# Optimization experiments

Hardware: AMD Instinct MI355X
Metric: run time of the kernel (lower is better)

Reference implementation:

```python
import jax, jax.numpy as jnp
import numpy as np

N = 50000        # n_nodes
E = 640000       # n_edges
D = 128          # d_model (in_dim == out_dim)
H = 8            # num_heads
DH = D // H      # head dim = 16
EPS = 1e-5


def _batchnorm(x, g, b):
    # BatchNorm1d, training-mode batch statistics (biased variance)
    mu = jnp.mean(x, axis=0)
    var = jnp.mean((x - mu) ** 2, axis=0)
    return (x - mu) * jax.lax.rsqrt(var + EPS) * g + b


def setup_inputs() -> dict:
    key = jax.random.key(0)
    ks = jax.random.split(key, 16)
    s = 0.05
    h = jax.random.normal(ks[0], (N, D), jnp.float32)
    src = jax.random.randint(ks[1], (E,), 0, N)
    # guarantee every node has >= 1 incoming edge (avoids z == 0)
    dst = jnp.concatenate([jnp.arange(N), jax.random.randint(ks[2], (E - N,), 0, N)])
    return {
        "h": h,
        "src": src,
        "dst": dst,
        "WQ": jax.random.normal(ks[3], (D, D), jnp.float32) * s,
        "WK": jax.random.normal(ks[4], (D, D), jnp.float32) * s,
        "WV": jax.random.normal(ks[5], (D, D), jnp.float32) * s,
        "WO": jax.random.normal(ks[6], (D, D), jnp.float32) * s,
        "bO": jnp.zeros((D,), jnp.float32),
        "W1": jax.random.normal(ks[7], (2 * D, D), jnp.float32) * s,
        "b1": jnp.zeros((2 * D,), jnp.float32),
        "W2": jax.random.normal(ks[8], (D, 2 * D), jnp.float32) * s,
        "b2": jnp.zeros((D,), jnp.float32),
        "bn1_g": jnp.ones((D,), jnp.float32),
        "bn1_b": jnp.zeros((D,), jnp.float32),
        "bn2_g": jnp.ones((D,), jnp.float32),
        "bn2_b": jnp.zeros((D,), jnp.float32),
    }


def reference(h, src, dst, WQ, WK, WV, WO, bO, W1, b1, W2, b2, bn1_g, bn1_b, bn2_g, bn2_b):
    n = h.shape[0]
    # projections -> [N, H, DH]
    Q = (h @ WQ.T).reshape(n, H, DH)
    K = (h @ WK.T).reshape(n, H, DH)
    V = (h @ WV.T).reshape(n, H, DH)
    # per-edge score: sum(K[src] * Q[dst]) -> [E, H]; clamp/exp (scaled_exp)
    score = jnp.sum(K[src] * Q[dst], axis=-1) / np.sqrt(DH)
    score = jnp.exp(jnp.clip(score, -5.0, 5.0))
    # scatter-sum weighted values and normalizers to destination nodes
    wV = jax.ops.segment_sum(V[src] * score[..., None], dst, num_segments=n)  # [N,H,DH]
    z = jax.ops.segment_sum(score, dst, num_segments=n)                       # [N,H]
    attn = (wV / z[..., None]).reshape(n, D)
    # O projection + residual + BN1
    h1 = _batchnorm(h + (attn @ WO.T + bO), bn1_g, bn1_b)
    # FFN + residual + BN2
    f = jax.nn.relu(h1 @ W1.T + b1) @ W2.T + b2
    return _batchnorm(h1 + f, bn2_g, bn2_b)
```

## Files before the change

### kernel.cpp

```cpp
#include <hip/hip_runtime.h>
#include <math.h>


#define ND128 16384
typedef _Float16 f16;
typedef __attribute__((ext_vector_type(8))) _Float16 h8;
typedef __attribute__((ext_vector_type(4))) _Float16 h4;
typedef __attribute__((ext_vector_type(2))) _Float16 h2;
typedef __attribute__((ext_vector_type(4))) float f4;
typedef __attribute__((ext_vector_type(2))) float ff2;

__device__ __forceinline__ ff2 fp8x2_dec(unsigned v) {
#if __has_builtin(__builtin_amdgcn_cvt_pk_f32_fp8)
    return __builtin_amdgcn_cvt_pk_f32_fp8((int)v, false);
#else
    ff2 r;
    unsigned b0 = v & 0xffu, b1 = (v >> 8) & 0xffu;
    {
        unsigned e = (b0 >> 3) & 15u, m = b0 & 7u;
        float x = e ? __uint_as_float(((e + 120u) << 23) | (m << 20)) : (float)m * 0.001953125f;
        r.x = (b0 & 0x80u) ? -x : x;
    }
    {
        unsigned e = (b1 >> 3) & 15u, m = b1 & 7u;
        float x = e ? __uint_as_float(((e + 120u) << 23) | (m << 20)) : (float)m * 0.001953125f;
        r.y = (b1 & 0x80u) ? -x : x;
    }
    return r;
#endif
}

__device__ __forceinline__ ff2 dec_lo(unsigned v) {
#if __has_builtin(__builtin_amdgcn_cvt_pk_f32_fp8)
    return __builtin_amdgcn_cvt_pk_f32_fp8((int)v, false);
#else
    return fp8x2_dec(v & 0xffffu);
#endif
}
__device__ __forceinline__ ff2 dec_hi(unsigned v) {
#if __has_builtin(__builtin_amdgcn_cvt_pk_f32_fp8)
    return __builtin_amdgcn_cvt_pk_f32_fp8((int)v, true);
#else
    return fp8x2_dec((v >> 16) & 0xffffu);
#endif
}

#if !__has_builtin(__builtin_amdgcn_cvt_pk_fp8_f32)
__device__ __forceinline__ unsigned char fp8_1(float f) {
    float a = fabsf(f);
    unsigned sg = (__float_as_uint(f) >> 31) << 7;
    if (a >= 448.f) return (unsigned char)(sg | 0x7E);
    if (a < 0.0009765625f) return (unsigned char)sg;
    int E; float m = frexpf(a, &E);
    if (E - 1 < -6) {
        int q = (int)rintf(a * 512.f);
        if (q > 7) return (unsigned char)(sg | 0x08);
        return (unsigned char)(sg | q);
    }
    int q = (int)rintf(m * 16.f);
    if (q == 16) { q = 8; E += 1; }
    int Ef = E - 1 + 7;
    if (Ef > 15) return (unsigned char)(sg | 0x7E);
    return (unsigned char)(sg | (Ef << 3) | (q - 8));
}
#endif

__device__ __forceinline__ unsigned fp8_pack4(float a0, float a1, float a2, float a3) {
#if __has_builtin(__builtin_amdgcn_cvt_pk_fp8_f32)
    int pk = __builtin_amdgcn_cvt_pk_fp8_f32(a0, a1, 0, false);
    pk = __builtin_amdgcn_cvt_pk_fp8_f32(a2, a3, pk, true);
    return (unsigned)pk;
#else
    return (unsigned)fp8_1(a0) | ((unsigned)fp8_1(a1) << 8) |
           ((unsigned)fp8_1(a2) << 16) | ((unsigned)fp8_1(a3) << 24);
#endif
}

__global__ __launch_bounds__(256) void k_prep(
    const float* __restrict__ h, f16* __restrict__ hb,
    const float* __restrict__ WQ, const float* __restrict__ WK,
    const float* __restrict__ WV, const float* __restrict__ WO,
    const float* __restrict__ W2,
    f16* __restrict__ Wqb, f16* __restrict__ Wkb,
    f16* __restrict__ Wvb, f16* __restrict__ Wob, f16* __restrict__ W2b,
    float* __restrict__ bn, int* __restrict__ cursor, int N)
{
    const int slab = blockIdx.x, my = blockIdx.y;
    const int tid = threadIdx.x;
    if (my == 0) {
        if (tid < 128) {
            int ci = slab * 128 + tid;
            if (ci < N) cursor[ci] = 0;
        }
        if (slab == 6) { bn[tid] = 0.f; bn[tid + 256] = 0.f; }
    }
#pragma unroll
    for (int it2 = 0; it2 < 4; ++it2) {
        int it = my * 4 + it2;
        int cid = it * 256 + tid;
        int lane = cid & 63;
        int m = (cid >> 6) & 7;
        int kb = cid >> 9;
        int row = slab * 128 + m * 16 + (lane & 15);
        int col = kb * 32 + (lane >> 4) * 8;
        f16 o8[8];
        if (row < N) {
            const float* p = h + (size_t)row * 128 + col;
            float4 f0 = *(const float4*)p;
            float4 f1 = *(const float4*)(p + 4);
            o8[0] = (f16)f0.x; o8[1] = (f16)f0.y; o8[2] = (f16)f0.z; o8[3] = (f16)f0.w;
            o8[4] = (f16)f1.x; o8[5] = (f16)f1.y; o8[6] = (f16)f1.z; o8[7] = (f16)f1.w;
        } else {
#pragma unroll
            for (int j = 0; j < 8; ++j) o8[j] = (f16)0.f;
        }
        *(h8*)(hb + (size_t)slab * ND128 + (size_t)cid * 8) = *(const h8*)o8;
    }
    if (slab < 6 && my == 1) {
        const float* Wsrc; f16* dst; int K, base;
        if (slab < 4) {
            Wsrc = slab == 0 ? WQ : slab == 1 ? WK : slab == 2 ? WV : WO;
            dst  = slab == 0 ? Wqb : slab == 1 ? Wkb : slab == 2 ? Wvb : Wob;
            K = 128; base = 0;
        } else {
            Wsrc = W2; dst = W2b; K = 256; base = (slab - 4) * 2048;
        }
#pragma unroll
        for (int it = 0; it < 8; ++it) {
            int cid = base + it * 256 + tid;
            int lane = cid & 63;
            int kb, nt;
            if (K == 128) { kb = (cid >> 6) & 3; nt = cid >> 8; }
            else          { kb = (cid >> 6) & 7; nt = cid >> 9; }
            int row = nt * 16 + (lane & 15);
            int col = kb * 32 + (lane >> 4) * 8;
            const float* p = Wsrc + (size_t)row * K + col;
            f16 o8[8];
#pragma unroll
            for (int j = 0; j < 8; ++j) o8[j] = (f16)p[j];
            *(h8*)(dst + (size_t)cid * 8) = *(const h8*)o8;
        }
    }
}

__global__ __launch_bounds__(256) void k_qkv(
    const f16* __restrict__ hb, const f16* __restrict__ Wqb,
    const f16* __restrict__ Wkb, const f16* __restrict__ Wvb,
    f16* __restrict__ Qb, unsigned char* __restrict__ Kb8,
    unsigned char* __restrict__ Vb8, int N)
{
    const int slab = blockIdx.x, oidx = blockIdx.y, mh = blockIdx.z;
    const int w = threadIdx.x >> 6, lane = threadIdx.x & 63;
    const f16* __restrict__ Wb = oidx == 0 ? Wqb : oidx == 1 ? Wkb : Wvb;
    const f16* A = hb + (size_t)slab * ND128;

    h8 bfr[2][4];
#pragma unroll
    for (int nt = 0; nt < 2; ++nt)
#pragma unroll
        for (int kb = 0; kb < 4; ++kb)
            bfr[nt][kb] = *(const h8*)(Wb + (size_t)(((2 * w + nt) * 4 + kb) * 64 + lane) * 8);

    f4 acc[4][2];
    f4 zero = {0.f, 0.f, 0.f, 0.f};
#pragma unroll
    for (int m = 0; m < 4; ++m) { acc[m][0] = zero; acc[m][1] = zero; }

#pragma unroll
    for (int m = 0; m < 4; ++m) {
        int mg = mh * 4 + m;
#pragma unroll
        for (int kb = 0; kb < 4; ++kb) {
            h8 a = *(const h8*)(A + (size_t)((kb * 8 + mg) * 64 + lane) * 8);
            acc[m][0] = __builtin_amdgcn_mfma_f32_16x16x32_f16(bfr[0][kb], a, acc[m][0], 0, 0, 0);
            acc[m][1] = __builtin_amdgcn_mfma_f32_16x16x32_f16(bfr[1][kb], a, acc[m][1], 0, 0, 0);
        }
    }

    const int rl = lane & 15, quad = lane >> 4;
    if (oidx == 0) {
#pragma unroll
        for (int m = 0; m < 4; ++m) {
            int gr = slab * 128 + (mh * 4 + m) * 16 + rl;
            if (gr < N) {
#pragma unroll
                for (int nt = 0; nt < 2; ++nt) {
                    h4 o;
                    o[0] = (f16)acc[m][nt][0]; o[1] = (f16)acc[m][nt][1];
                    o[2] = (f16)acc[m][nt][2]; o[3] = (f16)acc[m][nt][3];
                    *(h4*)(Qb + (size_t)gr * 128 + w * 32 + nt * 16 + quad * 4) = o;
                }
            }
        }
    } else {
        unsigned char* __restrict__ O8 = oidx == 1 ? Kb8 : Vb8;
#pragma unroll
        for (int m = 0; m < 4; ++m) {
            int gr = slab * 128 + (mh * 4 + m) * 16 + rl;
            if (gr < N) {
#pragma unroll
                for (int nt = 0; nt < 2; ++nt) {
                    unsigned pk = fp8_pack4(acc[m][nt][0], acc[m][nt][1],
                                            acc[m][nt][2], acc[m][nt][3]);
                    *(unsigned*)(O8 + (size_t)gr * 128 + w * 32 + nt * 16 + quad * 4) = pk;
                }
            }
        }
    }
}

__global__ __launch_bounds__(256) void k_hist(
    const int* __restrict__ dst, int* __restrict__ cursor, int E)
{
    int e = blockIdx.x * 256 + threadIdx.x;
    if (e < E) atomicAdd(&cursor[dst[e]], 1);
}

__global__ __launch_bounds__(256) void k_scanA(
    const int* __restrict__ cnt, int* __restrict__ bsum, int N)
{
    const int t = threadIdx.x;
    int base = blockIdx.x * 2048 + t * 8;
    int s = 0;
#pragma unroll
    for (int j = 0; j < 8; ++j) {
        int idx = base + j;
        if (idx < N) s += cnt[idx];
    }
#pragma unroll
    for (int off = 32; off; off >>= 1) s += __shfl_down(s, off, 64);
    __shared__ int ws4[4];
    if ((t & 63) == 0) ws4[t >> 6] = s;
    __syncthreads();
    if (t == 0) bsum[blockIdx.x] = ws4[0] + ws4[1] + ws4[2] + ws4[3];
}

__global__ __launch_bounds__(256) void k_scanC(
    const int* __restrict__ cnt, const int* __restrict__ bsum,
    int* __restrict__ rowptr, int* __restrict__ cursor, int N, int nsb)
{
    const int t = threadIdx.x, b = blockIdx.x;
    __shared__ int sboff;
    if (t == 0) {
        int r = 0;
        for (int i2 = 0; i2 < b; ++i2) r += bsum[i2];
        sboff = r;
    }
    if (t == 64 && b == nsb - 1) {
        int r = 0;
        for (int i2 = 0; i2 < nsb; ++i2) r += bsum[i2];
        rowptr[N] = r;
    }
    int base = b * 2048 + t * 8;
    int loc[8];
    int s = 0;
#pragma unroll
    for (int j = 0; j < 8; ++j) {
        int idx = base + j;
        loc[j] = (idx < N) ? cnt[idx] : 0;
        s += loc[j];
    }
    __shared__ int part[256];
    part[t] = s;
    __syncthreads();
    for (int off = 1; off < 256; off <<= 1) {
        int v = (t >= off) ? part[t - off] : 0;
        __syncthreads();
        part[t] += v;
        __syncthreads();
    }
    int run = sboff + (t ? part[t - 1] : 0);
#pragma unroll
    for (int j = 0; j < 8; ++j) {
        int idx = base + j;
        if (idx < N) { rowptr[idx] = run; cursor[idx] = run; run += loc[j]; }
    }
}

__global__ __launch_bounds__(256) void k_scatter(
    const int* __restrict__ src, const int* __restrict__ dst,
    int* __restrict__ cursor, int* __restrict__ csr_src, int E)
{
    int e = blockIdx.x * 256 + threadIdx.x;
    if (e < E) {
        int pos = atomicAdd(&cursor[dst[e]], 1);
        csr_src[pos] = src[e];
    }
}

__global__ __launch_bounds__(256) void k_attn(
    const f16* __restrict__ Qb, const unsigned char* __restrict__ Kb8,
    const unsigned char* __restrict__ Vb8,
    const int* __restrict__ rowptr, const int* __restrict__ csr_src,
    f16* __restrict__ attnf, int N)
{
    const int node = blockIdx.x * 4 + (threadIdx.x >> 6);
    const int lane = threadIdx.x & 63;
    if (node >= N) return;
    const int e = lane >> 3;
    const int hd = lane & 7;
    const int beg = rowptr[node], end = rowptr[node + 1];

    float q[16];
    {
        const h8* qp = (const h8*)(Qb + (size_t)node * 128 + hd * 16);
        h8 q0 = qp[0], q1 = qp[1];
#pragma unroll
        for (int j = 0; j < 8; ++j) { q[j] = (float)q0[j]; q[8 + j] = (float)q1[j]; }
    }

    float acc[16];
#pragma unroll
    for (int c = 0; c < 16; ++c) acc[c] = 0.f;
    float z = 0.f;

    for (int i = beg; i < end; i += 8) {
        int eidx = i + e;
        bool valid = eidx < end;
        int s = csr_src[valid ? eidx : end - 1];
        const uint4 kv = *(const uint4*)(Kb8 + (size_t)s * 128 + hd * 16);
        const uint4 vv = *(const uint4*)(Vb8 + (size_t)s * 128 + hd * 16);

        ff2 k0 = dec_lo(kv.x), k1 = dec_hi(kv.x), k2 = dec_lo(kv.y), k3 = dec_hi(kv.y);
        ff2 k4 = dec_lo(kv.z), k5 = dec_hi(kv.z), k6 = dec_lo(kv.w), k7 = dec_hi(kv.w);
        float pa = q[0] * k0.x, pb = q[1] * k0.y;
        pa = fmaf(q[2],  k1.x, pa); pb = fmaf(q[3],  k1.y, pb);
        pa = fmaf(q[4],  k2.x, pa); pb = fmaf(q[5],  k2.y, pb);
        pa = fmaf(q[6],  k3.x, pa); pb = fmaf(q[7],  k3.y, pb);
        pa = fmaf(q[8],  k4.x, pa); pb = fmaf(q[9],  k4.y, pb);
        pa = fmaf(q[10], k5.x, pa); pb = fmaf(q[11], k5.y, pb);
        pa = fmaf(q[12], k6.x, pa); pb = fmaf(q[13], k6.y, pb);
        pa = fmaf(q[14], k7.x, pa); pb = fmaf(q[15], k7.y, pb);
        float p = pa + pb;

        float sc = __expf(fminf(fmaxf(p * 0.25f, -5.f), 5.f));
        sc = valid ? sc : 0.f;
        z += sc;

        ff2 v0 = dec_lo(vv.x), v1 = dec_hi(vv.x), v2 = dec_lo(vv.y), v3 = dec_hi(vv.y);
        ff2 v4 = dec_lo(vv.z), v5 = dec_hi(vv.z), v6 = dec_lo(vv.w), v7 = dec_hi(vv.w);
        acc[0]  = fmaf(v0.x, sc, acc[0]);  acc[1]  = fmaf(v0.y, sc, acc[1]);
        acc[2]  = fmaf(v1.x, sc, acc[2]);  acc[3]  = fmaf(v1.y, sc, acc[3]);
        acc[4]  = fmaf(v2.x, sc, acc[4]);  acc[5]  = fmaf(v2.y, sc, acc[5]);
        acc[6]  = fmaf(v3.x, sc, acc[6]);  acc[7]  = fmaf(v3.y, sc, acc[7]);
        acc[8]  = fmaf(v4.x, sc, acc[8]);  acc[9]  = fmaf(v4.y, sc, acc[9]);
        acc[10] = fmaf(v5.x, sc, acc[10]); acc[11] = fmaf(v5.y, sc, acc[11]);
        acc[12] = fmaf(v6.x, sc, acc[12]); acc[13] = fmaf(v6.y, sc, acc[13]);
        acc[14] = fmaf(v7.x, sc, acc[14]); acc[15] = fmaf(v7.y, sc, acc[15]);
    }

#pragma unroll
    for (int c = 0; c < 16; ++c) {
        acc[c] += __shfl_xor(acc[c], 8, 64);
        acc[c] += __shfl_xor(acc[c], 16, 64);
        acc[c] += __shfl_xor(acc[c], 32, 64);
    }
    z += __shfl_xor(z, 8, 64);
    z += __shfl_xor(z, 16, 64);
    z += __shfl_xor(z, 32, 64);
    float inv = 1.f / z;

    if (e < 2) {
        h8 o;
#pragma unroll
        for (int j = 0; j < 8; ++j) o[j] = (f16)(acc[e * 8 + j] * inv);
        int slab = node >> 7, m = (node >> 4) & 7, lr = node & 15;
        int kb = hd >> 1;
        int quad2 = (hd & 1) * 2 + e;
        *(h8*)(attnf + (size_t)slab * ND128 +
               (size_t)(((kb * 8 + m) * 64 + lr + 16 * quad2) * 8)) = o;
    }
}

__global__ __launch_bounds__(256) void k_oproj(
    const f16* __restrict__ attnf, const f16* __restrict__ Wob,
    const float* __restrict__ h, const float* __restrict__ bO,
    f16* __restrict__ t1b, float* __restrict__ bn, int N)
{
    __shared__ float csum[128], csq[128];
    const int tid = threadIdx.x, slab = blockIdx.x, mh = blockIdx.y;
    const int w = tid >> 6, lane = tid & 63;
    if (tid < 128) { csum[tid] = 0.f; csq[tid] = 0.f; }
    __syncthreads();
    const f16* A = attnf + (size_t)slab * ND128;

    h8 bfr[2][4];
#pragma unroll
    for (int nt = 0; nt < 2; ++nt)
#pragma unroll
        for (int kb = 0; kb < 4; ++kb)
            bfr[nt][kb] = *(const h8*)(Wob + (size_t)(((2 * w + nt) * 4 + kb) * 64 + lane) * 8);

    f4 acc[4][2];
    f4 zero = {0.f, 0.f, 0.f, 0.f};
#pragma unroll
    for (int m = 0; m < 4; ++m) { acc[m][0] = zero; acc[m][1] = zero; }
#pragma unroll
    for (int m = 0; m < 4; ++m) {
        int mg = mh * 4 + m;
#pragma unroll
        for (int kb = 0; kb < 4; ++kb) {
            h8 a = *(const h8*)(A + (size_t)((kb * 8 + mg) * 64 + lane) * 8);
            acc[m][0] = __builtin_amdgcn_mfma_f32_16x16x32_f16(bfr[0][kb], a, acc[m][0], 0, 0, 0);
            acc[m][1] = __builtin_amdgcn_mfma_f32_16x16x32_f16(bfr[1][kb], a, acc[m][1], 0, 0, 0);
        }
    }

    const int rl = lane & 15, quad = lane >> 4;
    float4 bo[2];
#pragma unroll
    for (int nt = 0; nt < 2; ++nt)
        bo[nt] = *(const float4*)(bO + w * 32 + nt * 16 + quad * 4);
    float pcs[2][4], pcq[2][4];
#pragma unroll
    for (int nt = 0; nt < 2; ++nt)
#pragma unroll
        for (int r = 0; r < 4; ++r) { pcs[nt][r] = 0.f; pcq[nt][r] = 0.f; }

#pragma unroll
    for (int m = 0; m < 4; ++m) {
        int mg = mh * 4 + m;
        int gr = slab * 128 + mg * 16 + rl;
        if (gr < N) {
#pragma unroll
            for (int nt = 0; nt < 2; ++nt) {
                int col0 = w * 32 + nt * 16 + quad * 4;
                float4 hv = *(const float4*)(h + (size_t)gr * 128 + col0);
                float v0 = acc[m][nt][0] + hv.x + bo[nt].x;
                float v1 = acc[m][nt][1] + hv.y + bo[nt].y;
                float v2 = acc[m][nt][2] + hv.z + bo[nt].z;
                float v3 = acc[m][nt][3] + hv.w + bo[nt].w;
                h4 o; o[0] = (f16)v0; o[1] = (f16)v1; o[2] = (f16)v2; o[3] = (f16)v3;
                *(h4*)(t1b + (size_t)slab * ND128 +
                       (size_t)(((w * 8 + mg) * 64 + (nt * 2 + (quad >> 1)) * 16 + rl) * 8 +
                                (quad & 1) * 4)) = o;
                pcs[nt][0] += v0; pcq[nt][0] += v0 * v0;
                pcs[nt][1] += v1; pcq[nt][1] += v1 * v1;
                pcs[nt][2] += v2; pcq[nt][2] += v2 * v2;
                pcs[nt][3] += v3; pcq[nt][3] += v3 * v3;
            }
        }
    }
#pragma unroll
    for (int nt = 0; nt < 2; ++nt)
#pragma unroll
        for (int r = 0; r < 4; ++r) {
            float s = pcs[nt][r], q = pcq[nt][r];
            s += __shfl_xor(s, 8, 16); q += __shfl_xor(q, 8, 16);
            s += __shfl_xor(s, 4, 16); q += __shfl_xor(q, 4, 16);
            s += __shfl_xor(s, 2, 16); q += __shfl_xor(q, 2, 16);
            s += __shfl_xor(s, 1, 16); q += __shfl_xor(q, 1, 16);
            if (rl == 0) {
                int cl = w * 32 + nt * 16 + quad * 4 + r;
                atomicAdd(&csum[cl], s);
                atomicAdd(&csq[cl], q);
            }
        }
    __syncthreads();
    if (tid < 128) {
        atomicAdd(bn + tid, csum[tid]);
        atomicAdd(bn + 128 + tid, csq[tid]);
    }
}

__global__ __launch_bounds__(128) void k_fold1(
    const float* __restrict__ bn, const float* __restrict__ g1,
    const float* __restrict__ bb1, const float* __restrict__ W1,
    const float* __restrict__ b1, f16* __restrict__ W1b,
    float* __restrict__ badj, float* __restrict__ sfold,
    float* __restrict__ bfold, int N)
{
    const int o = blockIdx.x, i = threadIdx.x;
    float invN = 1.f / (float)N;
    float mu = bn[i] * invN;
    float var = bn[128 + i] * invN - mu * mu;
    float s = g1[i] * rsqrtf(var + 1e-5f);
    float bb = bb1[i] - mu * s;
    if (o == 0) { sfold[i] = s; bfold[i] = bb; }
    float wv = W1[(size_t)o * 128 + i];
    __shared__ float red[128];
    red[i] = wv * bb;
    const int nt = o >> 4, lanelow = o & 15;
    const int kb = i >> 5, quad = (i >> 3) & 3, j = i & 7;
    W1b[(size_t)(((nt * 4 + kb) * 64 + lanelow + 16 * quad) * 8 + j)] = (f16)(wv * s);
    __syncthreads();
#pragma unroll
    for (int off = 64; off; off >>= 1) {
        if (i < off) red[i] += red[i + off];
        __syncthreads();
    }
    if (i == 0) badj[o] = b1[o] + red[0];
}

__global__ __launch_bounds__(256) void k_ffn1(
    const f16* __restrict__ t1b, const f16* __restrict__ W1b,
    const float* __restrict__ badj, f16* __restrict__ ub, int N)
{
    const int slab = blockIdx.x, ch = blockIdx.y, mh = blockIdx.z;
    const int w = threadIdx.x >> 6, lane = threadIdx.x & 63;
    const f16* A = t1b + (size_t)slab * ND128;

    h8 bfr[2][4];
#pragma unroll
    for (int nt = 0; nt < 2; ++nt)
#pragma unroll
        for (int kb = 0; kb < 4; ++kb) {
            int ntg = ch * 8 + 2 * w + nt;
            bfr[nt][kb] = *(const h8*)(W1b + (size_t)((ntg * 4 + kb) * 64 + lane) * 8);
        }

    f4 acc[4][2];
    f4 zero = {0.f, 0.f, 0.f, 0.f};
#pragma unroll
    for (int m = 0; m < 4; ++m) { acc[m][0] = zero; acc[m][1] = zero; }
#pragma unroll
    for (int m = 0; m < 4; ++m) {
        int mg = mh * 4 + m;
#pragma unroll
        for (int kb = 0; kb < 4; ++kb) {
            h8 a = *(const h8*)(A + (size_t)((kb * 8 + mg) * 64 + lane) * 8);
            acc[m][0] = __builtin_amdgcn_mfma_f32_16x16x32_f16(bfr[0][kb], a, acc[m][0], 0, 0, 0);
            acc[m][1] = __builtin_amdgcn_mfma_f32_16x16x32_f16(bfr[1][kb], a, acc[m][1], 0, 0, 0);
        }
    }

    const int rl = lane & 15, quad = lane >> 4;
    const int kbu = ch * 4 + w;
    float4 ba[2];
#pragma unroll
    for (int nt = 0; nt < 2; ++nt)
        ba[nt] = *(const float4*)(badj + ch * 128 + w * 32 + nt * 16 + quad * 4);
#pragma unroll
    for (int m = 0; m < 4; ++m) {
        int mg = mh * 4 + m;
        int gr = slab * 128 + mg * 16 + rl;
        if (gr < N) {
#pragma unroll
            for (int nt = 0; nt < 2; ++nt) {
                h4 o;
                o[0] = (f16)fmaxf(acc[m][nt][0] + ba[nt].x, 0.f);
                o[1] = (f16)fmaxf(acc[m][nt][1] + ba[nt].y, 0.f);
                o[2] = (f16)fmaxf(acc[m][nt][2] + ba[nt].z, 0.f);
                o[3] = (f16)fmaxf(acc[m][nt][3] + ba[nt].w, 0.f);
                *(h4*)(ub + (size_t)slab * 32768 +
                       (size_t)(((kbu * 8 + mg) * 64 + (nt * 2 + (quad >> 1)) * 16 + rl) * 8 +
                                (quad & 1) * 4)) = o;
            }
        }
    }
}

__global__ __launch_bounds__(256) void k_ffn2(
    const f16* __restrict__ ub, const f16* __restrict__ W2b,
    const f16* __restrict__ t1b,
    const float* __restrict__ sfold, const float* __restrict__ bfold,
    const float* __restrict__ b2, float* __restrict__ out,
    float* __restrict__ bn, int N)
{
    __shared__ float csum[128], csq[128], sS[128], sB[128];
    const int tid = threadIdx.x, slab = blockIdx.x, mh = blockIdx.y;
    const int w = tid >> 6, lane = tid & 63;
    if (tid < 128) {
        csum[tid] = 0.f; csq[tid] = 0.f;
        sS[tid] = sfold[tid]; sB[tid] = bfold[tid] + b2[tid];
    }
    __syncthreads();
    const f16* A = ub + (size_t)slab * 32768;
    const f16* T1 = t1b + (size_t)slab * ND128;

    h8 bfr[2][8];
#pragma unroll
    for (int nt = 0; nt < 2; ++nt)
#pragma unroll
        for (int kb = 0; kb < 8; ++kb)
            bfr[nt][kb] = *(const h8*)(W2b + (size_t)(((2 * w + nt) * 8 + kb) * 64 + lane) * 8);

    f4 acc[4][2];
    f4 zero = {0.f, 0.f, 0.f, 0.f};
#pragma unroll
    for (int m = 0; m < 4; ++m) { acc[m][0] = zero; acc[m][1] = zero; }
#pragma unroll
    for (int m = 0; m < 4; ++m) {
        int mg = mh * 4 + m;
#pragma unroll
        for (int kb = 0; kb < 8; ++kb) {
            h8 a = *(const h8*)(A + (size_t)((kb * 8 + mg) * 64 + lane) * 8);
            acc[m][0] = __builtin_amdgcn_mfma_f32_16x16x32_f16(bfr[0][kb], a, acc[m][0], 0, 0, 0);
            acc[m][1] = __builtin_amdgcn_mfma_f32_16x16x32_f16(bfr[1][kb], a, acc[m][1], 0, 0, 0);
        }
    }

    const int rl = lane & 15, quad = lane >> 4;
    float pcs[2][4], pcq[2][4];
#pragma unroll
    for (int nt = 0; nt < 2; ++nt)
#pragma unroll
        for (int r = 0; r < 4; ++r) { pcs[nt][r] = 0.f; pcq[nt][r] = 0.f; }

#pragma unroll
    for (int m = 0; m < 4; ++m) {
        int mg = mh * 4 + m;
        int gr = slab * 128 + mg * 16 + rl;
        if (gr < N) {
#pragma unroll
            for (int nt = 0; nt < 2; ++nt) {
                int col0 = w * 32 + nt * 16 + quad * 4;
                h4 t1v = *(const h4*)(T1 +
                    (size_t)(((w * 8 + mg) * 64 + (nt * 2 + (quad >> 1)) * 16 + rl) * 8 +
                             (quad & 1) * 4));
                float4 ss = *(const float4*)&sS[col0];
                float4 sb = *(const float4*)&sB[col0];
                float4 o;
                o.x = acc[m][nt][0] + fmaf(ss.x, (float)t1v[0], sb.x);
                o.y = acc[m][nt][1] + fmaf(ss.y, (float)t1v[1], sb.y);
                o.z = acc[m][nt][2] + fmaf(ss.z, (float)t1v[2], sb.z);
                o.w = acc[m][nt][3] + fmaf(ss.w, (float)t1v[3], sb.w);
                *(float4*)(out + (size_t)gr * 128 + col0) = o;
                pcs[nt][0] += o.x; pcq[nt][0] += o.x * o.x;
                pcs[nt][1] += o.y; pcq[nt][1] += o.y * o.y;
                pcs[nt][2] += o.z; pcq[nt][2] += o.z * o.z;
                pcs[nt][3] += o.w; pcq[nt][3] += o.w * o.w;
            }
        }
    }
#pragma unroll
    for (int nt = 0; nt < 2; ++nt)
#pragma unroll
        for (int r = 0; r < 4; ++r) {
            float s = pcs[nt][r], q = pcq[nt][r];
            s += __shfl_xor(s, 8, 16); q += __shfl_xor(q, 8, 16);
            s += __shfl_xor(s, 4, 16); q += __shfl_xor(q, 4, 16);
            s += __shfl_xor(s, 2, 16); q += __shfl_xor(q, 2, 16);
            s += __shfl_xor(s, 1, 16); q += __shfl_xor(q, 1, 16);
            if (rl == 0) {
                int cl = w * 32 + nt * 16 + quad * 4 + r;
                atomicAdd(&csum[cl], s);
                atomicAdd(&csq[cl], q);
            }
        }
    __syncthreads();
    if (tid < 128) {
        atomicAdd(bn + 256 + tid, csum[tid]);
        atomicAdd(bn + 384 + tid, csq[tid]);
    }
}

__global__ __launch_bounds__(256) void k_bn2(
    float* __restrict__ out, const float* __restrict__ bn,
    const float* __restrict__ g2, const float* __restrict__ bb2, int N)
{
    __shared__ float sS[128], sB[128];
    const int tid = threadIdx.x;
    if (tid < 128) {
        float invN = 1.f / (float)N;
        float mu = bn[256 + tid] * invN;
        float var = bn[384 + tid] * invN - mu * mu;
        float scl = g2[tid] * rsqrtf(var + 1e-5f);
        sS[tid] = scl;
        sB[tid] = bb2[tid] - mu * scl;
    }
    __syncthreads();
    size_t idx = (size_t)blockIdx.x * 256 + tid;
    size_t total = (size_t)N * 32;
    if (idx < total) {
        int c0 = (int)((idx * 4) & 127);
        float4 v = *(const float4*)(out + idx * 4);
        v.x = fmaf(v.x, sS[c0 + 0], sB[c0 + 0]);
        v.y = fmaf(v.y, sS[c0 + 1], sB[c0 + 1]);
        v.z = fmaf(v.z, sS[c0 + 2], sB[c0 + 2]);
        v.w = fmaf(v.w, sS[c0 + 3], sB[c0 + 3]);
        *(float4*)(out + idx * 4) = v;
    }
}

extern "C" void kernel_launch(void* const* d_in, const int* in_sizes, int n_in,
                              void* d_out, int out_size, void* d_ws, size_t ws_size,
                              hipStream_t stream)
{
    const float* h   = (const float*)d_in[0];
    const int*   src = (const int*)d_in[1];
    const int*   dst = (const int*)d_in[2];
    const float* WQ  = (const float*)d_in[3];
    const float* WK  = (const float*)d_in[4];
    const float* WV  = (const float*)d_in[5];
    const float* WO  = (const float*)d_in[6];
    const float* bO  = (const float*)d_in[7];
    const float* W1  = (const float*)d_in[8];
    const float* b1  = (const float*)d_in[9];
    const float* W2  = (const float*)d_in[10];
    const float* b2  = (const float*)d_in[11];
    const float* g1  = (const float*)d_in[12];
    const float* bb1 = (const float*)d_in[13];
    const float* g2  = (const float*)d_in[14];
    const float* bb2 = (const float*)d_in[15];
    float* out = (float*)d_out;

    int N = in_sizes[0] / 128;
    int E = in_sizes[1];
    const int slabs = (N + 127) / 128;
    const int nsb = (N + 2047) / 2048;
    const size_t B1 = (size_t)slabs * 32768;

    char* Wp = (char*)d_ws;
    f16* hb  = (f16*)Wp;
    f16* Qb  = (f16*)(Wp + B1);
    unsigned char* Kb8 = (unsigned char*)(Wp + 2 * B1);
    unsigned char* Vb8 = (unsigned char*)(Wp + 2 * B1 + B1 / 2);
    f16* ub  = (f16*)(Wp + B1);
    f16* t1b = (f16*)(Wp + 3 * B1);
    const size_t base = 4 * B1;
    f16* Wqb = (f16*)(Wp + base);
    f16* Wkb = (f16*)(Wp + base + 32768);
    f16* Wvb = (f16*)(Wp + base + 65536);
    f16* Wob = (f16*)(Wp + base + 98304);
    f16* W1b = (f16*)(Wp + base + 131072);
    f16* W2b = (f16*)(Wp + base + 196608);
    float* badj  = (float*)(Wp + base + 262144);
    float* sfold = (float*)(Wp + base + 263168);
    float* bfold = (float*)(Wp + base + 263680);
    float* bn    = (float*)(Wp + base + 264192);
    int* cursor  = (int*)(Wp + base + 266240);
    int* rowptr  = (int*)(Wp + base + 266240 + (size_t)N * 4);
    int* csr     = (int*)(Wp + base + 266240 + (size_t)N * 8 + 8);
    int* bsum    = (int*)((char*)csr + (size_t)E * 4);

    k_prep<<<dim3(slabs, 2), 256, 0, stream>>>(h, hb, WQ, WK, WV, WO, W2,
                                               Wqb, Wkb, Wvb, Wob, W2b, bn, cursor, N);
    k_qkv<<<dim3(slabs, 3, 2), 256, 0, stream>>>(hb, Wqb, Wkb, Wvb, Qb, Kb8, Vb8, N);
    k_hist<<<(E + 255) / 256, 256, 0, stream>>>(dst, cursor, E);
    k_scanA<<<nsb, 256, 0, stream>>>(cursor, bsum, N);
    k_scanC<<<nsb, 256, 0, stream>>>(cursor, bsum, rowptr, cursor, N, nsb);
    k_scatter<<<(E + 255) / 256, 256, 0, stream>>>(src, dst, cursor, csr, E);
    k_attn<<<(N + 3) / 4, 256, 0, stream>>>(Qb, Kb8, Vb8, rowptr, csr, hb, N);
    k_oproj<<<dim3(slabs, 2), 256, 0, stream>>>(hb, Wob, h, bO, t1b, bn, N);
    k_fold1<<<256, 128, 0, stream>>>(bn, g1, bb1, W1, b1, W1b, badj, sfold, bfold, N);
    k_ffn1<<<dim3(slabs, 2, 2), 256, 0, stream>>>(t1b, W1b, badj, ub, N);
    k_ffn2<<<dim3(slabs, 2), 256, 0, stream>>>(ub, W2b, t1b, sfold, bfold, b2, out, bn, N);
    k_bn2<<<(int)(((size_t)N * 32 + 255) / 256), 256, 0, stream>>>(out, bn, g2, bb2, N);
}
```

Baseline: 327.4 us.

## Store K/V in fp16 and restructure attention to one edge per wave

K and V are now stored as fp16 instead of fp8, so the attention kernel no longer has to decode fp8. The attention kernel is reorganized so that each lane owns two head-dim channels. Edges are processed one at a time per wave, unrolled by four, using fdot2, DPP reductions within each 8-lane head group, exp2 with the scale folded into Q, and packed fp16 accumulation of V. This doubles the K/V gather bytes and accumulates in fp16, which may cost precision, in exchange for fewer instructions, no cross-lane shuffle reduction at the end, and coalesced 256-byte row reads per edge.

```diff
diff --git a/kernel.cpp b/kernel.cpp
--- a/kernel.cpp
+++ b/kernel.cpp
@@ -8,72 +8,33 @@
 typedef __attribute__((ext_vector_type(4))) _Float16 h4;
 typedef __attribute__((ext_vector_type(2))) _Float16 h2;
 typedef __attribute__((ext_vector_type(4))) float f4;
-typedef __attribute__((ext_vector_type(2))) float ff2;
-
-__device__ __forceinline__ ff2 fp8x2_dec(unsigned v) {
-#if __has_builtin(__builtin_amdgcn_cvt_pk_f32_fp8)
-    return __builtin_amdgcn_cvt_pk_f32_fp8((int)v, false);
+
+__device__ __forceinline__ float fdot2h(h2 a, h2 b) {
+#if __has_builtin(__builtin_amdgcn_fdot2)
+    return __builtin_amdgcn_fdot2(a, b, 0.f, false);
 #else
-    ff2 r;
-    unsigned b0 = v & 0xffu, b1 = (v >> 8) & 0xffu;
-    {
-        unsigned e = (b0 >> 3) & 15u, m = b0 & 7u;
-        float x = e ? __uint_as_float(((e + 120u) << 23) | (m << 20)) : (float)m * 0.001953125f;
-        r.x = (b0 & 0x80u) ? -x : x;
-    }
-    {
-        unsigned e = (b1 >> 3) & 15u, m = b1 & 7u;
-        float x = e ? __uint_as_float(((e + 120u) << 23) | (m << 20)) : (float)m * 0.001953125f;
-        r.y = (b1 & 0x80u) ? -x : x;
-    }
-    return r;
+    return (float)a[0] * (float)b[0] + (float)a[1] * (float)b[1];
 #endif
 }
 
-__device__ __forceinline__ ff2 dec_lo(unsigned v) {
-#if __has_builtin(__builtin_amdgcn_cvt_pk_f32_fp8)
-    return __builtin_amdgcn_cvt_pk_f32_fp8((int)v, false);
+__device__ __forceinline__ float fast_exp2(float x) {
+#if __has_builtin(__builtin_amdgcn_exp2f)
+    return __builtin_amdgcn_exp2f(x);
 #else
-    return fp8x2_dec(v & 0xffffu);
+    return exp2f(x);
 #endif
 }
-__device__ __forceinline__ ff2 dec_hi(unsigned v) {
-#if __has_builtin(__builtin_amdgcn_cvt_pk_f32_fp8)
-    return __builtin_amdgcn_cvt_pk_f32_fp8((int)v, true);
-#else
-    return fp8x2_dec((v >> 16) & 0xffffu);
-#endif
-}
-
-#if !__has_builtin(__builtin_amdgcn_cvt_pk_fp8_f32)
-__device__ __forceinline__ unsigned char fp8_1(float f) {
-    float a = fabsf(f);
-    unsigned sg = (__float_as_uint(f) >> 31) << 7;
-    if (a >= 448.f) return (unsigned char)(sg | 0x7E);
-    if (a < 0.0009765625f) return (unsigned char)sg;
-    int E; float m = frexpf(a, &E);
-    if (E - 1 < -6) {
-        int q = (int)rintf(a * 512.f);
-        if (q > 7) return (unsigned char)(sg | 0x08);
-        return (unsigned char)(sg | q);
-    }
-    int q = (int)rintf(m * 16.f);
-    if (q == 16) { q = 8; E += 1; }
-    int Ef = E - 1 + 7;
-    if (Ef > 15) return (unsigned char)(sg | 0x7E);
-    return (unsigned char)(sg | (Ef << 3) | (q - 8));
-}
-#endif
-
-__device__ __forceinline__ unsigned fp8_pack4(float a0, float a1, float a2, float a3) {
-#if __has_builtin(__builtin_amdgcn_cvt_pk_fp8_f32)
-    int pk = __builtin_amdgcn_cvt_pk_fp8_f32(a0, a1, 0, false);
-    pk = __builtin_amdgcn_cvt_pk_fp8_f32(a2, a3, pk, true);
-    return (unsigned)pk;
-#else
-    return (unsigned)fp8_1(a0) | ((unsigned)fp8_1(a1) << 8) |
-           ((unsigned)fp8_1(a2) << 16) | ((unsigned)fp8_1(a3) << 24);
-#endif
+
+template <int CTRL>
+__device__ __forceinline__ float dppadd(float x) {
+    int t = __builtin_amdgcn_update_dpp(0, __float_as_int(x), CTRL, 0xF, 0xF, false);
+    return x + __int_as_float(t);
+}
+__device__ __forceinline__ float wsum8(float p) {
+    p = dppadd<0xB1>(p);
+    p = dppadd<0x4E>(p);
+    p = dppadd<0x141>(p);
+    return p;
 }
 
 __global__ __launch_bounds__(256) void k_prep(
@@ -146,12 +107,13 @@
 __global__ __launch_bounds__(256) void k_qkv(
     const f16* __restrict__ hb, const f16* __restrict__ Wqb,
     const f16* __restrict__ Wkb, const f16* __restrict__ Wvb,
-    f16* __restrict__ Qb, unsigned char* __restrict__ Kb8,
-    unsigned char* __restrict__ Vb8, int N)
+    f16* __restrict__ Qb, f16* __restrict__ Kh,
+    f16* __restrict__ Vh, int N)
 {
     const int slab = blockIdx.x, oidx = blockIdx.y, mh = blockIdx.z;
     const int w = threadIdx.x >> 6, lane = threadIdx.x & 63;
     const f16* __restrict__ Wb = oidx == 0 ? Wqb : oidx == 1 ? Wkb : Wvb;
+    f16* __restrict__ Ob = oidx == 0 ? Qb : oidx == 1 ? Kh : Vh;
     const f16* A = hb + (size_t)slab * ND128;
 
     h8 bfr[2][4];
@@ -178,32 +140,16 @@
     }
 
     const int rl = lane & 15, quad = lane >> 4;
-    if (oidx == 0) {
-#pragma unroll
-        for (int m = 0; m < 4; ++m) {
-            int gr = slab * 128 + (mh * 4 + m) * 16 + rl;
-            if (gr < N) {
-#pragma unroll
-                for (int nt = 0; nt < 2; ++nt) {
-                    h4 o;
-                    o[0] = (f16)acc[m][nt][0]; o[1] = (f16)acc[m][nt][1];
-                    o[2] = (f16)acc[m][nt][2]; o[3] = (f16)acc[m][nt][3];
-                    *(h4*)(Qb + (size_t)gr * 128 + w * 32 + nt * 16 + quad * 4) = o;
-                }
-            }
-        }
-    } else {
-        unsigned char* __restrict__ O8 = oidx == 1 ? Kb8 : Vb8;
-#pragma unroll
-        for (int m = 0; m < 4; ++m) {
-            int gr = slab * 128 + (mh * 4 + m) * 16 + rl;
-            if (gr < N) {
-#pragma unroll
-                for (int nt = 0; nt < 2; ++nt) {
-                    unsigned pk = fp8_pack4(acc[m][nt][0], acc[m][nt][1],
-                                            acc[m][nt][2], acc[m][nt][3]);
-                    *(unsigned*)(O8 + (size_t)gr * 128 + w * 32 + nt * 16 + quad * 4) = pk;
-                }
+#pragma unroll
+    for (int m = 0; m < 4; ++m) {
+        int gr = slab * 128 + (mh * 4 + m) * 16 + rl;
+        if (gr < N) {
+#pragma unroll
+            for (int nt = 0; nt < 2; ++nt) {
+                h4 o;
+                o[0] = (f16)acc[m][nt][0]; o[1] = (f16)acc[m][nt][1];
+                o[2] = (f16)acc[m][nt][2]; o[3] = (f16)acc[m][nt][3];
+                *(h4*)(Ob + (size_t)gr * 128 + w * 32 + nt * 16 + quad * 4) = o;
             }
         }
     }
@@ -289,87 +235,83 @@
 }
 
 __global__ __launch_bounds__(256) void k_attn(
-    const f16* __restrict__ Qb, const unsigned char* __restrict__ Kb8,
-    const unsigned char* __restrict__ Vb8,
+    const f16* __restrict__ Qb, const f16* __restrict__ Kh,
+    const f16* __restrict__ Vh,
     const int* __restrict__ rowptr, const int* __restrict__ csr_src,
     f16* __restrict__ attnf, int N)
 {
     const int node = blockIdx.x * 4 + (threadIdx.x >> 6);
     const int lane = threadIdx.x & 63;
     if (node >= N) return;
-    const int e = lane >> 3;
-    const int hd = lane & 7;
     const int beg = rowptr[node], end = rowptr[node + 1];
 
-    float q[16];
+    h2 qs;
     {
-        const h8* qp = (const h8*)(Qb + (size_t)node * 128 + hd * 16);
-        h8 q0 = qp[0], q1 = qp[1];
-#pragma unroll
-        for (int j = 0; j < 8; ++j) { q[j] = (float)q0[j]; q[8 + j] = (float)q1[j]; }
-    }
-
-    float acc[16];
-#pragma unroll
-    for (int c = 0; c < 16; ++c) acc[c] = 0.f;
+        h2 q2 = ((const h2*)(Qb + (size_t)node * 128))[lane];
+        const float SCL = 0.25f * 1.44269504f;
+        qs[0] = (f16)((float)q2[0] * SCL);
+        qs[1] = (f16)((float)q2[1] * SCL);
+    }
+    const float CLP = 5.f * 1.44269504f;
+
+    const h2* __restrict__ K2 = (const h2*)Kh;
+    const h2* __restrict__ V2 = (const h2*)Vh;
+
+    h2 accA, accB;
+    accA[0] = (f16)0.f; accA[1] = (f16)0.f;
+    accB[0] = (f16)0.f; accB[1] = (f16)0.f;
     float z = 0.f;
 
-    for (int i = beg; i < end; i += 8) {
-        int eidx = i + e;
-        bool valid = eidx < end;
-        int s = csr_src[valid ? eidx : end - 1];
-        const uint4 kv = *(const uint4*)(Kb8 + (size_t)s * 128 + hd * 16);
-        const uint4 vv = *(const uint4*)(Vb8 + (size_t)s * 128 + hd * 16);
-
-        ff2 k0 = dec_lo(kv.x), k1 = dec_hi(kv.x), k2 = dec_lo(kv.y), k3 = dec_hi(kv.y);
-        ff2 k4 = dec_lo(kv.z), k5 = dec_hi(kv.z), k6 = dec_lo(kv.w), k7 = dec_hi(kv.w);
-        float pa = q[0] * k0.x, pb = q[1] * k0.y;
-        pa = fmaf(q[2],  k1.x, pa); pb = fmaf(q[3],  k1.y, pb);
-        pa = fmaf(q[4],  k2.x, pa); pb = fmaf(q[5],  k2.y, pb);
-        pa = fmaf(q[6],  k3.x, pa); pb = fmaf(q[7],  k3.y, pb);
-        pa = fmaf(q[8],  k4.x, pa); pb = fmaf(q[9],  k4.y, pb);
-        pa = fmaf(q[10], k5.x, pa); pb = fmaf(q[11], k5.y, pb);
-        pa = fmaf(q[12], k6.x, pa); pb = fmaf(q[13], k6.y, pb);
-        pa = fmaf(q[14], k7.x, pa); pb = fmaf(q[15], k7.y, pb);
-        float p = pa + pb;
-
-        float sc = __expf(fminf(fmaxf(p * 0.25f, -5.f), 5.f));
-        sc = valid ? sc : 0.f;
-        z += sc;
-
-        ff2 v0 = dec_lo(vv.x), v1 = dec_hi(vv.x), v2 = dec_lo(vv.y), v3 = dec_hi(vv.y);
-        ff2 v4 = dec_lo(vv.z), v5 = dec_hi(vv.z), v6 = dec_lo(vv.w), v7 = dec_hi(vv.w);
-        acc[0]  = fmaf(v0.x, sc, acc[0]);  acc[1]  = fmaf(v0.y, sc, acc[1]);
-        acc[2]  = fmaf(v1.x, sc, acc[2]);  acc[3]  = fmaf(v1.y, sc, acc[3]);
-        acc[4]  = fmaf(v2.x, sc, acc[4]);  acc[5]  = fmaf(v2.y, sc, acc[5]);
-        acc[6]  = fmaf(v3.x, sc, acc[6]);  acc[7]  = fmaf(v3.y, sc, acc[7]);
-        acc[8]  = fmaf(v4.x, sc, acc[8]);  acc[9]  = fmaf(v4.y, sc, acc[9]);
-        acc[10] = fmaf(v5.x, sc, acc[10]); acc[11] = fmaf(v5.y, sc, acc[11]);
-        acc[12] = fmaf(v6.x, sc, acc[12]); acc[13] = fmaf(v6.y, sc, acc[13]);
-        acc[14] = fmaf(v7.x, sc, acc[14]); acc[15] = fmaf(v7.y, sc, acc[15]);
-    }
-
-#pragma unroll
-    for (int c = 0; c < 16; ++c) {
-        acc[c] += __shfl_xor(acc[c], 8, 64);
-        acc[c] += __shfl_xor(acc[c], 16, 64);
-        acc[c] += __shfl_xor(acc[c], 32, 64);
-    }
-    z += __shfl_xor(z, 8, 64);
-    z += __shfl_xor(z, 16, 64);
-    z += __shfl_xor(z, 32, 64);
+    int i = beg;
+    for (; i + 3 < end; i += 4) {
+        int s0 = csr_src[i], s1 = csr_src[i + 1];
+        int s2 = csr_src[i + 2], s3 = csr_src[i + 3];
+        h2 k0 = K2[(size_t)s0 * 64 + lane];
+        h2 k1 = K2[(size_t)s1 * 64 + lane];
+        h2 k2 = K2[(size_t)s2 * 64 + lane];
+        h2 k3 = K2[(size_t)s3 * 64 + lane];
+        h2 v0 = V2[(size_t)s0 * 64 + lane];
+        h2 v1 = V2[(size_t)s1 * 64 + lane];
+        h2 v2 = V2[(size_t)s2 * 64 + lane];
+        h2 v3 = V2[(size_t)s3 * 64 + lane];
+        float p0 = fdot2h(qs, k0);
+        float p1 = fdot2h(qs, k1);
+        float p2 = fdot2h(qs, k2);
+        float p3 = fdot2h(qs, k3);
+        p0 = wsum8(p0); p1 = wsum8(p1); p2 = wsum8(p2); p3 = wsum8(p3);
+        float sc0 = fast_exp2(fminf(fmaxf(p0, -CLP), CLP));
+        float sc1 = fast_exp2(fminf(fmaxf(p1, -CLP), CLP));
+        float sc2 = fast_exp2(fminf(fmaxf(p2, -CLP), CLP));
+        float sc3 = fast_exp2(fminf(fmaxf(p3, -CLP), CLP));
+        z += sc0 + sc1 + sc2 + sc3;
+        h2 c0; c0[0] = (f16)sc0; c0[1] = (f16)sc0;
+        h2 c1; c1[0] = (f16)sc1; c1[1] = (f16)sc1;
+        h2 c2; c2[0] = (f16)sc2; c2[1] = (f16)sc2;
+        h2 c3; c3[0] = (f16)sc3; c3[1] = (f16)sc3;
+        accA += c0 * v0; accB += c1 * v1;
+        accA += c2 * v2; accB += c3 * v3;
+    }
+    for (; i < end; ++i) {
+        int s0 = csr_src[i];
+        h2 k0 = K2[(size_t)s0 * 64 + lane];
+        h2 v0 = V2[(size_t)s0 * 64 + lane];
+        float p0 = fdot2h(qs, k0);
+        p0 = wsum8(p0);
+        float sc0 = fast_exp2(fminf(fmaxf(p0, -CLP), CLP));
+        z += sc0;
+        h2 c0; c0[0] = (f16)sc0; c0[1] = (f16)sc0;
+        accA += c0 * v0;
+    }
+
     float inv = 1.f / z;
-
-    if (e < 2) {
-        h8 o;
-#pragma unroll
-        for (int j = 0; j < 8; ++j) o[j] = (f16)(acc[e * 8 + j] * inv);
-        int slab = node >> 7, m = (node >> 4) & 7, lr = node & 15;
-        int kb = hd >> 1;
-        int quad2 = (hd & 1) * 2 + e;
-        *(h8*)(attnf + (size_t)slab * ND128 +
-               (size_t)(((kb * 8 + m) * 64 + lr + 16 * quad2) * 8)) = o;
-    }
+    float ax = ((float)accA[0] + (float)accB[0]) * inv;
+    float ay = ((float)accA[1] + (float)accB[1]) * inv;
+    h2 o2;
+    o2[0] = (f16)ax; o2[1] = (f16)ay;
+    int slab = node >> 7, m = (node >> 4) & 7, lr = node & 15;
+    int kb = lane >> 4, quad2 = (lane & 15) >> 2, j = (lane & 3) * 2;
+    *(h2*)(attnf + (size_t)slab * ND128 +
+           (size_t)(((kb * 8 + m) * 64 + lr + 16 * quad2) * 8 + j)) = o2;
 }
 
 __global__ __launch_bounds__(256) void k_oproj(
@@ -704,8 +646,8 @@
     char* Wp = (char*)d_ws;
     f16* hb  = (f16*)Wp;
     f16* Qb  = (f16*)(Wp + B1);
-    unsigned char* Kb8 = (unsigned char*)(Wp + 2 * B1);
-    unsigned char* Vb8 = (unsigned char*)(Wp + 2 * B1 + B1 / 2);
+    f16* Kh  = (f16*)(Wp + 2 * B1);
+    f16* Vh  = (f16*)(Wp + 3 * B1);
     f16* ub  = (f16*)(Wp + B1);
     f16* t1b = (f16*)(Wp + 3 * B1);
     const size_t base = 4 * B1;
@@ -726,12 +668,12 @@
 
     k_prep<<<dim3(slabs, 2), 256, 0, stream>>>(h, hb, WQ, WK, WV, WO, W2,
                                                Wqb, Wkb, Wvb, Wob, W2b, bn, cursor, N);
-    k_qkv<<<dim3(slabs, 3, 2), 256, 0, stream>>>(hb, Wqb, Wkb, Wvb, Qb, Kb8, Vb8, N);
+    k_qkv<<<dim3(slabs, 3, 2), 256, 0, stream>>>(hb, Wqb, Wkb, Wvb, Qb, Kh, Vh, N);
     k_hist<<<(E + 255) / 256, 256, 0, stream>>>(dst, cursor, E);
     k_scanA<<<nsb, 256, 0, stream>>>(cursor, bsum, N);
     k_scanC<<<nsb, 256, 0, stream>>>(cursor, bsum, rowptr, cursor, N, nsb);
     k_scatter<<<(E + 255) / 256, 256, 0, stream>>>(src, dst, cursor, csr, E);
-    k_attn<<<(N + 3) / 4, 256, 0, stream>>>(Qb, Kb8, Vb8, rowptr, csr, hb, N);
+    k_attn<<<(N + 3) / 4, 256, 0, stream>>>(Qb, Kh, Vh, rowptr, csr, hb, N);
     k_oproj<<<dim3(slabs, 2), 256, 0, stream>>>(hb, Wob, h, bO, t1b, bn, N);
     k_fold1<<<256, 128, 0, stream>>>(bn, g1, bb1, W1, b1, W1b, badj, sfold, bfold, N);
     k_ffn1<<<dim3(slabs, 2, 2), 256, 0, stream>>>(t1b, W1b, badj, ub, N);
```

New measurement: 329.0 us. Within noise of the previous version (+0.5%).
